# Kernel tuning notes

Measured on AMD Instinct MI355X. Metric: run time of the kernel, lower is better.

Reference implementation:

```python
import jax, jax.numpy as jnp
import numpy as np

B, S, D, H = 2, 2048, 1024, 16
DK = D // H
NEG = -1e9


def setup_inputs() -> dict:
    key = jax.random.key(0)
    ks = jax.random.split(key, 12)
    inp = {
        "query": jax.random.normal(ks[0], (B, S, D), jnp.float32),
        "key": jax.random.normal(ks[1], (B, S, D), jnp.float32),
        "value": jax.random.normal(ks[2], (B, S, D), jnp.float32),
        "mask": jax.random.randint(ks[3], (B, S), 0, 2, jnp.int32),
    }
    # 4 linears (q, k, v, out), each d_model x d_model with bias.
    scale = 1.0 / np.sqrt(D)
    for i, name in enumerate(["wq", "wk", "wv", "wo"]):
        inp[name] = jax.random.uniform(ks[4 + i], (D, D), jnp.float32, -scale, scale)
        inp["b" + name[1]] = jax.random.uniform(ks[8 + i], (D,), jnp.float32, -scale, scale)
    return inp


def _split_heads(x):  # [B,S,D] -> [B,H,S,DK]
    return x.reshape(B, S, H, DK).transpose(0, 2, 1, 3)


def reference(query, key, value, mask, wq, bq, wk, bk, wv, bv, wo, bo):
    q = _split_heads(query @ wq.T + bq)
    k = _split_heads(key @ wk.T + bk)
    v = _split_heads(value @ wv.T + bv)
    scores = jnp.einsum("bhqd,bhkd->bhqk", q, k) / jnp.sqrt(jnp.float32(DK))
    # mask: [B,S] -> [B,1,1,S]; masked_fill where mask == 0
    m = mask[:, None, None, :]
    scores = jnp.where(m == 0, NEG, scores)
    attn = jax.nn.softmax(scores, axis=-1)  # dropout p=0 (eval) -> identity
    x = jnp.einsum("bhqk,bhkd->bhqd", attn, v)
    x = x.transpose(0, 2, 1, 3).reshape(B, S, D)
    return x @ wo.T + bo
```

## Files before the change

### kernel.cpp

```cpp
#include <hip/hip_runtime.h>


typedef _Float16 f16;
typedef _Float16 f16x8 __attribute__((ext_vector_type(8)));
typedef _Float16 f16x4 __attribute__((ext_vector_type(4)));
typedef __fp16 fp16x2r __attribute__((ext_vector_type(2)));
typedef float f32x4 __attribute__((ext_vector_type(4)));

#define MFMA_F16(a, b, c) __builtin_amdgcn_mfma_f32_16x16x32_f16((a), (b), (c), 0, 0, 0)
#define L2E 1.44269504088896340736f

__device__ __forceinline__ void gld16(const void* g, void* l) {
    __builtin_amdgcn_global_load_lds(
        (__attribute__((address_space(1))) void*)(g),
        (__attribute__((address_space(3))) void*)(l), 16, 0, 0);
}

__global__ __launch_bounds__(256) void cvt_kernel(
    const float* __restrict__ q, const float* __restrict__ k,
    const float* __restrict__ v,
    const float* __restrict__ wq, const float* __restrict__ wk,
    const float* __restrict__ wv, const float* __restrict__ wo,
    f16* __restrict__ oq, f16* __restrict__ ok, f16* __restrict__ ov,
    f16* __restrict__ owq, f16* __restrict__ owk, f16* __restrict__ owv,
    f16* __restrict__ owo)
{
    const int z = blockIdx.y;
    const float* src;
    f16* dst;
    int n;
    switch (z) {
        case 0: src = q;  dst = oq;  n = 4194304; break;
        case 1: src = k;  dst = ok;  n = 4194304; break;
        case 2: src = v;  dst = ov;  n = 4194304; break;
        case 3: src = wq; dst = owq; n = 1048576; break;
        case 4: src = wk; dst = owk; n = 1048576; break;
        case 5: src = wv; dst = owv; n = 1048576; break;
        default: src = wo; dst = owo; n = 1048576; break;
    }
    int idx = (blockIdx.x * 256 + threadIdx.x) * 8;
    if (idx >= n) return;
    float4 a = *(const float4*)(src + idx);
    float4 b = *(const float4*)(src + idx + 4);
    f16x8 h = { (f16)a.x, (f16)a.y, (f16)a.z, (f16)a.w,
                (f16)b.x, (f16)b.y, (f16)b.z, (f16)b.w };
    *(f16x8*)(dst + idx) = h;
}

__device__ __forceinline__ void stage_qkv(
    const f16* __restrict__ P0, const f16* __restrict__ P1,
    int blockM, int blockN, int k0, f16* Ad, f16* Bd,
    int wave, int srow2, int schunk)
{
#pragma unroll
    for (int p = 0; p < 2; p++) {
        int r0 = wave * 32 + p * 16;
        gld16(&P0[(size_t)(blockM + r0 + srow2) * 1024 + k0 + schunk * 8],
              &Ad[r0 * 32]);
        gld16(&P1[(size_t)(blockN + r0 + srow2) * 1024 + k0 + schunk * 8],
              &Bd[r0 * 32]);
    }
}

__global__ __launch_bounds__(256) void proj_qkv_kernel(
    const f16* __restrict__ xq, const f16* __restrict__ xk,
    const f16* __restrict__ xv,
    const f16* __restrict__ wqh, const f16* __restrict__ wkh,
    const f16* __restrict__ wvh,
    const float* __restrict__ bq, const float* __restrict__ bk,
    const float* __restrict__ bv,
    f16* __restrict__ qh, f16* __restrict__ kh, f16* __restrict__ vt)
{
    const int z = blockIdx.z;
    const f16* X = (z == 0) ? xq : (z == 1) ? xk : xv;
    const f16* W = (z == 0) ? wqh : (z == 1) ? wkh : wvh;
    const float* bias = (z == 0) ? bq : (z == 1) ? bk : bv;
    const f16* P0 = (z < 2) ? W : X;
    const f16* P1 = (z < 2) ? X : W;

    __shared__ __align__(16) f16 smem[24576];
    f16* L = smem;

    const int t = threadIdx.x;
    const int wave = t >> 6, lane = t & 63, quad = lane >> 4, l15 = lane & 15;
    const int m_base = (wave >> 1) * 64, n_base = (wave & 1) * 64;
    const int blockM = (z < 2) ? blockIdx.y * 128 : blockIdx.x * 128;
    const int blockN = (z < 2) ? blockIdx.x * 128 : blockIdx.y * 128;

    const int srow2 = lane >> 2;
    const int schunk = (lane & 3) ^ ((srow2 >> 1) & 3);
    const int rchunk = (l15 >> 1) & 3;

    f32x4 acc[4][4];
#pragma unroll
    for (int mt = 0; mt < 4; mt++)
#pragma unroll
        for (int nt = 0; nt < 4; nt++)
            acc[mt][nt] = (f32x4){0.f, 0.f, 0.f, 0.f};

    f16 *Ac = smem,          *An = smem + 4096,  *Af = smem + 8192;
    f16 *Bc = smem + 12288,  *Bn = smem + 16384, *Bf = smem + 20480;

    stage_qkv(P0, P1, blockM, blockN, 0,  Ac, Bc, wave, srow2, schunk);
    stage_qkv(P0, P1, blockM, blockN, 32, An, Bn, wave, srow2, schunk);
    asm volatile("s_waitcnt vmcnt(4)" ::: "memory");

    for (int ki = 0; ki < 32; ki++) {
        __builtin_amdgcn_s_barrier();
        __builtin_amdgcn_sched_barrier(0);
        if (ki < 30)
            stage_qkv(P0, P1, blockM, blockN, (ki + 2) * 32, Af, Bf,
                      wave, srow2, schunk);

        f16x8 af[4], bf[4];
#pragma unroll
        for (int mt = 0; mt < 4; mt++)
            af[mt] = *(const f16x8*)(&Ac[(m_base + mt * 16 + l15) * 32 +
                                         ((quad ^ rchunk) << 3)]);
#pragma unroll
        for (int nt = 0; nt < 4; nt++)
            bf[nt] = *(const f16x8*)(&Bc[(n_base + nt * 16 + l15) * 32 +
                                         ((quad ^ rchunk) << 3)]);
        __builtin_amdgcn_s_setprio(1);
#pragma unroll
        for (int mt = 0; mt < 4; mt++)
#pragma unroll
            for (int nt = 0; nt < 4; nt++)
                acc[mt][nt] = MFMA_F16(af[mt], bf[nt], acc[mt][nt]);
        __builtin_amdgcn_s_setprio(0);

        if (ki < 30)
            asm volatile("s_waitcnt vmcnt(4)" ::: "memory");
        else if (ki == 30)
            asm volatile("s_waitcnt vmcnt(0)" ::: "memory");
        f16* tA = Ac; Ac = An; An = Af; Af = tA;
        f16* tB = Bc; Bc = Bn; Bn = Bf; Bf = tB;
    }

    if (z < 2) {
        f16* o = (z == 0) ? qh : kh;
        const float scale = (z == 0) ? 0.125f * L2E : 1.0f;
        float4 b4[4];
#pragma unroll
        for (int mt = 0; mt < 4; mt++)
            b4[mt] = *(const float4*)(&bias[blockM + m_base + mt * 16 + quad * 4]);

#pragma unroll
        for (int half = 0; half < 2; half++) {
            __syncthreads();
            if ((wave & 1) == half) {
#pragma unroll
                for (int mt = 0; mt < 4; mt++)
#pragma unroll
                    for (int nt = 0; nt < 4; nt++) {
                        f16x4 pk = {
                            (f16)((acc[mt][nt][0] + b4[mt].x) * scale),
                            (f16)((acc[mt][nt][1] + b4[mt].y) * scale),
                            (f16)((acc[mt][nt][2] + b4[mt].z) * scale),
                            (f16)((acc[mt][nt][3] + b4[mt].w) * scale) };
                        *(f16x4*)(&L[(nt * 16 + l15) * 136 +
                                     m_base + mt * 16 + quad * 4]) = pk;
                    }
            }
            __syncthreads();
#pragma unroll
            for (int pass = 0; pass < 4; pass++) {
                int unit = pass * 32 + (t >> 3);
                int hh = unit >> 6, s_loc = unit & 63;
                f16x8 vv = *(const f16x8*)(&L[s_loc * 136 + hh * 64 + (t & 7) * 8]);
                int s_glob = blockN + half * 64 + s_loc;
                int b = s_glob >> 11, s = s_glob & 2047;
                int h_glob = (blockM >> 6) + hh;
                *(f16x8*)(&o[(((size_t)(b * 16 + h_glob) * 2048 + s) << 6) +
                             (t & 7) * 8]) = vv;
            }
        }
    } else {
        float bv_[4];
#pragma unroll
        for (int nt = 0; nt < 4; nt++)
            bv_[nt] = bias[blockN + n_base + nt * 16 + l15];

#pragma unroll
        for (int half = 0; half < 2; half++) {
            __syncthreads();
            if ((wave & 1) == half) {
#pragma unroll
                for (int mt = 0; mt < 4; mt++)
#pragma unroll
                    for (int nt = 0; nt < 4; nt++) {
                        f16x4 pk = { (f16)(acc[mt][nt][0] + bv_[nt]),
                                     (f16)(acc[mt][nt][1] + bv_[nt]),
                                     (f16)(acc[mt][nt][2] + bv_[nt]),
                                     (f16)(acc[mt][nt][3] + bv_[nt]) };
                        *(f16x4*)(&L[(nt * 16 + l15) * 136 +
                                     m_base + mt * 16 + quad * 4]) = pk;
                    }
            }
            __syncthreads();
#pragma unroll
            for (int pass = 0; pass < 4; pass++) {
                int f_loc = pass * 16 + (t >> 4);
                int tt = t & 15;
                int bb = (tt >= 8) ? 64 : 0;
                int o  = (tt & 7) * 8;
                int p  = (o >> 5) & 1;
                int c  = (o >> 3) & 3;
                int g1 = bb + p * 32 + c * 4;
                const f16* Lrow = &L[f_loc * 136];
                f16x4 lo = *(const f16x4*)(&Lrow[g1]);
                f16x4 hi = *(const f16x4*)(&Lrow[g1 + 16]);
                f16x8 vv = __builtin_shufflevector(lo, hi, 0, 1, 2, 3, 4, 5, 6, 7);
                int feat = blockN + half * 64 + f_loc;
                int hh = feat >> 6, dk = feat & 63;
                int b = blockM >> 11;
                int s0 = (blockM & 2047) + bb + o;
                *(f16x8*)(&vt[((size_t)((b * 16 + hh) * 64 + dk) << 11) + s0]) = vv;
            }
        }
    }
}

__device__ __forceinline__ void flash_stage2(
    const f16* kbase, const f16* vbase, int key0,
    f16* Kb, f16* Vb, int wg, int srow8, int sblk)
{
#pragma unroll
    for (int p = 0; p < 2; p++) {
        int r0 = wg * 16 + p * 8;
        int row = r0 + srow8;
        gld16(&kbase[(size_t)(key0 + row) * 64 + sblk * 8], &Kb[r0 * 64]);
        gld16(&vbase[(size_t)row * 2048 + key0 + sblk * 8], &Vb[r0 * 64]);
    }
}

__device__ __forceinline__ void flash_phase2(
    const f16* Kbuf, const f16* Vbuf, const float* bias_all, int key0,
    const f16x8 (&qf)[2][2], int quad, int l15,
    f32x4 (&O)[2][4], f32x4 (&lacc)[2])
{
    const int sw = l15 & 7;
    f32x4 sc[2][4];
#pragma unroll
    for (int nt = 0; nt < 4; nt++) {
        const f16* krow = &Kbuf[(nt * 16 + l15) * 64];
        f16x8 kf0 = *(const f16x8*)(&krow[(quad ^ sw) << 3]);
        f16x8 kf1 = *(const f16x8*)(&krow[((quad + 4) ^ sw) << 3]);
        float4 b4 = *(const float4*)(&bias_all[key0 + nt * 16 + quad * 4]);
        __builtin_amdgcn_s_setprio(1);
#pragma unroll
        for (int cb = 0; cb < 2; cb++) {
            f32x4 z4 = (f32x4){b4.x, b4.y, b4.z, b4.w};
            z4 = MFMA_F16(kf0, qf[cb][0], z4);
            sc[cb][nt] = MFMA_F16(kf1, qf[cb][1], z4);
        }
        __builtin_amdgcn_s_setprio(0);
    }
    const f16x8 ones8 = {(f16)1.f, (f16)1.f, (f16)1.f, (f16)1.f,
                         (f16)1.f, (f16)1.f, (f16)1.f, (f16)1.f};
    union P8u { f16x8 v8; fp16x2r h[4]; };
    P8u pp[2][2];
#pragma unroll
    for (int cb = 0; cb < 2; cb++) {
#pragma unroll
        for (int nt = 0; nt < 4; nt++) {
            float p0 = __builtin_amdgcn_exp2f(sc[cb][nt][0]);
            float p1 = __builtin_amdgcn_exp2f(sc[cb][nt][1]);
            float p2 = __builtin_amdgcn_exp2f(sc[cb][nt][2]);
            float p3 = __builtin_amdgcn_exp2f(sc[cb][nt][3]);
            pp[cb][nt >> 1].h[(nt & 1) * 2 + 0] = __builtin_amdgcn_cvt_pkrtz(p0, p1);
            pp[cb][nt >> 1].h[(nt & 1) * 2 + 1] = __builtin_amdgcn_cvt_pkrtz(p2, p3);
        }
        lacc[cb] = MFMA_F16(ones8, pp[cb][0].v8, lacc[cb]);
        lacc[cb] = MFMA_F16(ones8, pp[cb][1].v8, lacc[cb]);
    }
    __builtin_amdgcn_s_setprio(1);
#pragma unroll
    for (int nto = 0; nto < 4; nto++) {
        const f16* vrow = &Vbuf[(nto * 16 + l15) * 64];
        f16x8 va = *(const f16x8*)(&vrow[(quad ^ sw) << 3]);
        f16x8 vb = *(const f16x8*)(&vrow[((4 + quad) ^ sw) << 3]);
#pragma unroll
        for (int cb = 0; cb < 2; cb++) {
            O[cb][nto] = MFMA_F16(va, pp[cb][0].v8, O[cb][nto]);
            O[cb][nto] = MFMA_F16(vb, pp[cb][1].v8, O[cb][nto]);
        }
    }
    __builtin_amdgcn_s_setprio(0);
}

__global__
__attribute__((amdgpu_flat_work_group_size(512, 512)))
__attribute__((amdgpu_waves_per_eu(4, 4)))
void flash_kernel(
    const f16* __restrict__ qh, const f16* __restrict__ kh,
    const f16* __restrict__ vt, const int* __restrict__ mask,
    f16* __restrict__ ctx)
{
    __shared__ __align__(16) f16 KV[8 * 4096];
    __shared__ float bias_all[2048];

    const int t = threadIdx.x;
    const int wave = t >> 6, lane = t & 63, quad = lane >> 4, l15 = lane & 15;
    const int group = wave >> 2, wg = wave & 3;
    const int bh = blockIdx.x;
    const int b = bh >> 4, h = bh & 15;
    const int q0 = blockIdx.y * 128;

    const f16* qbase = qh + (size_t)bh * (2048 * 64);
    const f16* kbase = kh + (size_t)bh * (2048 * 64);
    const f16* vbase = vt + (size_t)bh * (64 * 2048);

    f16* K0 = &KV[((0 * 2 + group) * 2 + 0) * 4096];
    f16* V0 = &KV[((0 * 2 + group) * 2 + 1) * 4096];
    f16* K1 = &KV[((1 * 2 + group) * 2 + 0) * 4096];
    f16* V1 = &KV[((1 * 2 + group) * 2 + 1) * 4096];

#pragma unroll
    for (int j = 0; j < 4; j++) {
        int i = j * 512 + t;
        bias_all[i] = (mask[b * 2048 + i] == 0) ? -1.0e9f : 0.0f;
    }

    f16x8 qf[2][2];
#pragma unroll
    for (int cb = 0; cb < 2; cb++) {
        int qrow = q0 + wg * 32 + cb * 16 + l15;
        qf[cb][0] = *(const f16x8*)(&qbase[qrow * 64 + quad * 8]);
        qf[cb][1] = *(const f16x8*)(&qbase[qrow * 64 + 32 + quad * 8]);
    }

    f32x4 O[2][4];
#pragma unroll
    for (int cb = 0; cb < 2; cb++)
#pragma unroll
        for (int n = 0; n < 4; n++) O[cb][n] = (f32x4){0.f, 0.f, 0.f, 0.f};
    f32x4 lacc[2] = {(f32x4){0.f, 0.f, 0.f, 0.f}, (f32x4){0.f, 0.f, 0.f, 0.f}};

    const int srow8 = lane >> 3;
    const int sblk = (lane & 7) ^ srow8;

    flash_stage2(kbase, vbase, group * 64, K0, V0, wg, srow8, sblk);

    for (int k2 = 0; k2 < 16; k2 += 2) {
        __syncthreads();
        flash_stage2(kbase, vbase, (k2 + 1) * 128 + group * 64, K1, V1,
                     wg, srow8, sblk);
        flash_phase2(K0, V0, bias_all, k2 * 128 + group * 64,
                     qf, quad, l15, O, lacc);
        __syncthreads();
        if (k2 < 14)
            flash_stage2(kbase, vbase, (k2 + 2) * 128 + group * 64, K0, V0,
                         wg, srow8, sblk);
        flash_phase2(K1, V1, bias_all, (k2 + 1) * 128 + group * 64,
                     qf, quad, l15, O, lacc);
    }

    __syncthreads();
    float* Red = (float*)KV;
    const int t4 = wg * 64 + lane;
    if (group == 1) {
#pragma unroll
        for (int cb = 0; cb < 2; cb++) {
#pragma unroll
            for (int nto = 0; nto < 4; nto++)
                *(f32x4*)(&Red[(cb * 4 + nto) * 1024 + t4 * 4]) = O[cb][nto];
            Red[8 * 1024 + cb * 256 + t4] = lacc[cb][0];
        }
    }
    __syncthreads();
    if (group == 0) {
#pragma unroll
        for (int cb = 0; cb < 2; cb++) {
            const float l2 = Red[8 * 1024 + cb * 256 + t4];
            const float inv_l = 1.0f / (lacc[cb][0] + l2);
            int qrow = q0 + wg * 32 + cb * 16 + l15;
#pragma unroll
            for (int nto = 0; nto < 4; nto++) {
                f32x4 o2 = *(const f32x4*)(&Red[(cb * 4 + nto) * 1024 + t4 * 4]);
                f16x4 pk = { (f16)((O[cb][nto][0] + o2[0]) * inv_l),
                             (f16)((O[cb][nto][1] + o2[1]) * inv_l),
                             (f16)((O[cb][nto][2] + o2[2]) * inv_l),
                             (f16)((O[cb][nto][3] + o2[3]) * inv_l) };
                *(f16x4*)(&ctx[(size_t)(b * 2048 + qrow) * 1024 + h * 64 +
                               nto * 16 + quad * 4]) = pk;
            }
        }
    }
}

__device__ __forceinline__ void stage_out(
    const f16* __restrict__ ctx, const f16* __restrict__ woh,
    int blockM, int blockN, int k0, f16* Ad, f16* Bd,
    int wave, int srow2, int schunk)
{
#pragma unroll
    for (int p = 0; p < 2; p++) {
        int r0 = wave * 32 + p * 16;
        gld16(&ctx[(size_t)(blockM + r0 + srow2) * 1024 + k0 + schunk * 8],
              &Ad[r0 * 32]);
    }
    {
        int r0 = wave * 16;
        gld16(&woh[(size_t)(blockN + r0 + srow2) * 1024 + k0 + schunk * 8],
              &Bd[r0 * 32]);
    }
}

__global__ __launch_bounds__(256) void proj_out_kernel(
    const f16* __restrict__ ctx, const f16* __restrict__ woh,
    const float* __restrict__ bo, float* __restrict__ out)
{
    __shared__ __align__(16) f16 smem[18432];

    const int t = threadIdx.x;
    const int wave = t >> 6, lane = t & 63, quad = lane >> 4, l15 = lane & 15;
    const int m_base = (wave >> 1) * 64, n_base = (wave & 1) * 32;
    const int blockM = blockIdx.x * 128;
    const int blockN = blockIdx.y * 64;

    const int srow2 = lane >> 2;
    const int schunk = (lane & 3) ^ ((srow2 >> 1) & 3);
    const int rchunk = (l15 >> 1) & 3;

    f32x4 acc[4][2];
#pragma unroll
    for (int mt = 0; mt < 4; mt++)
#pragma unroll
        for (int nt = 0; nt < 2; nt++)
            acc[mt][nt] = (f32x4){0.f, 0.f, 0.f, 0.f};

    f16 *Ac = smem,          *An = smem + 4096,  *Af = smem + 8192;
    f16 *Bc = smem + 12288,  *Bn = smem + 14336, *Bf = smem + 16384;

    stage_out(ctx, woh, blockM, blockN, 0,  Ac, Bc, wave, srow2, schunk);
    stage_out(ctx, woh, blockM, blockN, 32, An, Bn, wave, srow2, schunk);
    asm volatile("s_waitcnt vmcnt(3)" ::: "memory");

    for (int ki = 0; ki < 32; ki++) {
        __builtin_amdgcn_s_barrier();
        __builtin_amdgcn_sched_barrier(0);
        if (ki < 30)
            stage_out(ctx, woh, blockM, blockN, (ki + 2) * 32, Af, Bf,
                      wave, srow2, schunk);

        f16x8 af[4], bf[2];
#pragma unroll
        for (int mt = 0; mt < 4; mt++)
            af[mt] = *(const f16x8*)(&Ac[(m_base + mt * 16 + l15) * 32 +
                                         ((quad ^ rchunk) << 3)]);
#pragma unroll
        for (int nt = 0; nt < 2; nt++)
            bf[nt] = *(const f16x8*)(&Bc[(n_base + nt * 16 + l15) * 32 +
                                         ((quad ^ rchunk) << 3)]);
        __builtin_amdgcn_s_setprio(1);
#pragma unroll
        for (int mt = 0; mt < 4; mt++)
#pragma unroll
            for (int nt = 0; nt < 2; nt++)
                acc[mt][nt] = MFMA_F16(af[mt], bf[nt], acc[mt][nt]);
        __builtin_amdgcn_s_setprio(0);

        if (ki < 30)
            asm volatile("s_waitcnt vmcnt(3)" ::: "memory");
        else if (ki == 30)
            asm volatile("s_waitcnt vmcnt(0)" ::: "memory");
        f16* tA = Ac; Ac = An; An = Af; Af = tA;
        f16* tB = Bc; Bc = Bn; Bn = Bf; Bf = tB;
    }

    float bo_[2];
#pragma unroll
    for (int nt = 0; nt < 2; nt++)
        bo_[nt] = bo[blockN + n_base + nt * 16 + l15];

#pragma unroll
    for (int mt = 0; mt < 4; mt++) {
        int row0 = blockM + m_base + mt * 16 + quad * 4;
#pragma unroll
        for (int nt = 0; nt < 2; nt++) {
            int col_g = blockN + n_base + nt * 16 + l15;
#pragma unroll
            for (int i = 0; i < 4; i++)
                out[(size_t)(row0 + i) * 1024 + col_g] = acc[mt][nt][i] + bo_[nt];
        }
    }
}

extern "C" void kernel_launch(void* const* d_in, const int* in_sizes, int n_in,
                              void* d_out, int out_size, void* d_ws, size_t ws_size,
                              hipStream_t stream) {
    const float* query = (const float*)d_in[0];
    const float* key_  = (const float*)d_in[1];
    const float* value = (const float*)d_in[2];
    const int*   mask  = (const int*)d_in[3];
    const float* wq = (const float*)d_in[4];
    const float* bq = (const float*)d_in[5];
    const float* wk = (const float*)d_in[6];
    const float* bk = (const float*)d_in[7];
    const float* wv = (const float*)d_in[8];
    const float* bv = (const float*)d_in[9];
    const float* wo = (const float*)d_in[10];
    const float* bo = (const float*)d_in[11];
    float* out = (float*)d_out;

    f16* xq  = (f16*)d_ws;
    f16* xk  = xq  + 4194304;
    f16* xv  = xk  + 4194304;
    f16* wqh = xv  + 4194304;
    f16* wkh = wqh + 1048576;
    f16* wvh = wkh + 1048576;
    f16* woh = wvh + 1048576;
    f16* qh  = woh + 1048576;
    f16* kh  = qh  + 4194304;
    f16* vt  = kh  + 4194304;
    f16* ctx = xq;

    cvt_kernel<<<dim3(2048, 7), 256, 0, stream>>>(
        query, key_, value, wq, wk, wv, wo, xq, xk, xv, wqh, wkh, wvh, woh);
    proj_qkv_kernel<<<dim3(32, 8, 3), 256, 0, stream>>>(
        xq, xk, xv, wqh, wkh, wvh, bq, bk, bv, qh, kh, vt);
    flash_kernel<<<dim3(32, 16), 512, 0, stream>>>(qh, kh, vt, mask, ctx);
    proj_out_kernel<<<dim3(32, 16), 256, 0, stream>>>(ctx, woh, bo, out);
}
```

Before: 209.6 us.

## Replace MFMA row-sum with scalar accumulation and retile output projection

```diff
diff --git a/kernel.cpp b/kernel.cpp
--- a/kernel.cpp
+++ b/kernel.cpp
@@ -237,7 +237,7 @@
 __device__ __forceinline__ void flash_phase2(
     const f16* Kbuf, const f16* Vbuf, const float* bias_all, int key0,
     const f16x8 (&qf)[2][2], int quad, int l15,
-    f32x4 (&O)[2][4], f32x4 (&lacc)[2])
+    f32x4 (&O)[2][4], float (&lsum)[2])
 {
     const int sw = l15 & 7;
     f32x4 sc[2][4];
@@ -256,12 +256,11 @@
         }
         __builtin_amdgcn_s_setprio(0);
     }
-    const f16x8 ones8 = {(f16)1.f, (f16)1.f, (f16)1.f, (f16)1.f,
-                         (f16)1.f, (f16)1.f, (f16)1.f, (f16)1.f};
     union P8u { f16x8 v8; fp16x2r h[4]; };
     P8u pp[2][2];
 #pragma unroll
     for (int cb = 0; cb < 2; cb++) {
+        float lacc = 0.f;
 #pragma unroll
         for (int nt = 0; nt < 4; nt++) {
             float p0 = __builtin_amdgcn_exp2f(sc[cb][nt][0]);
@@ -270,9 +269,9 @@
             float p3 = __builtin_amdgcn_exp2f(sc[cb][nt][3]);
             pp[cb][nt >> 1].h[(nt & 1) * 2 + 0] = __builtin_amdgcn_cvt_pkrtz(p0, p1);
             pp[cb][nt >> 1].h[(nt & 1) * 2 + 1] = __builtin_amdgcn_cvt_pkrtz(p2, p3);
-        }
-        lacc[cb] = MFMA_F16(ones8, pp[cb][0].v8, lacc[cb]);
-        lacc[cb] = MFMA_F16(ones8, pp[cb][1].v8, lacc[cb]);
+            lacc += (p0 + p1) + (p2 + p3);
+        }
+        lsum[cb] += lacc;
     }
     __builtin_amdgcn_s_setprio(1);
 #pragma unroll
@@ -335,7 +334,7 @@
     for (int cb = 0; cb < 2; cb++)
 #pragma unroll
         for (int n = 0; n < 4; n++) O[cb][n] = (f32x4){0.f, 0.f, 0.f, 0.f};
-    f32x4 lacc[2] = {(f32x4){0.f, 0.f, 0.f, 0.f}, (f32x4){0.f, 0.f, 0.f, 0.f}};
+    float lsum[2] = {0.f, 0.f};
 
     const int srow8 = lane >> 3;
     const int sblk = (lane & 7) ^ srow8;
@@ -347,13 +346,21 @@
         flash_stage2(kbase, vbase, (k2 + 1) * 128 + group * 64, K1, V1,
                      wg, srow8, sblk);
         flash_phase2(K0, V0, bias_all, k2 * 128 + group * 64,
-                     qf, quad, l15, O, lacc);
+                     qf, quad, l15, O, lsum);
         __syncthreads();
         if (k2 < 14)
             flash_stage2(kbase, vbase, (k2 + 2) * 128 + group * 64, K0, V0,
                          wg, srow8, sblk);
         flash_phase2(K1, V1, bias_all, (k2 + 1) * 128 + group * 64,
-                     qf, quad, l15, O, lacc);
+                     qf, quad, l15, O, lsum);
+    }
+
+#pragma unroll
+    for (int cb = 0; cb < 2; cb++) {
+        float v = lsum[cb];
+        v += __shfl_xor(v, 16, 64);
+        v += __shfl_xor(v, 32, 64);
+        lsum[cb] = v;
     }
 
     __syncthreads();
@@ -365,7 +372,7 @@
 #pragma unroll
             for (int nto = 0; nto < 4; nto++)
                 *(f32x4*)(&Red[(cb * 4 + nto) * 1024 + t4 * 4]) = O[cb][nto];
-            Red[8 * 1024 + cb * 256 + t4] = lacc[cb][0];
+            Red[8 * 1024 + cb * 256 + t4] = lsum[cb];
         }
     }
     __syncthreads();
@@ -373,7 +380,7 @@
 #pragma unroll
         for (int cb = 0; cb < 2; cb++) {
             const float l2 = Red[8 * 1024 + cb * 256 + t4];
-            const float inv_l = 1.0f / (lacc[cb][0] + l2);
+            const float inv_l = 1.0f / (lsum[cb] + l2);
             int qrow = q0 + wg * 32 + cb * 16 + l15;
 #pragma unroll
             for (int nto = 0; nto < 4; nto++) {
@@ -392,18 +399,15 @@
 __device__ __forceinline__ void stage_out(
     const f16* __restrict__ ctx, const f16* __restrict__ woh,
     int blockM, int blockN, int k0, f16* Ad, f16* Bd,
-    int wave, int srow2, int schunk)
+    int wave, int srow8, int sblk)
 {
 #pragma unroll
     for (int p = 0; p < 2; p++) {
-        int r0 = wave * 32 + p * 16;
-        gld16(&ctx[(size_t)(blockM + r0 + srow2) * 1024 + k0 + schunk * 8],
-              &Ad[r0 * 32]);
-    }
-    {
-        int r0 = wave * 16;
-        gld16(&woh[(size_t)(blockN + r0 + srow2) * 1024 + k0 + schunk * 8],
-              &Bd[r0 * 32]);
+        int r0 = wave * 16 + p * 8;
+        gld16(&ctx[(size_t)(blockM + r0 + srow8) * 1024 + k0 + sblk * 8],
+              &Ad[r0 * 64]);
+        gld16(&woh[(size_t)(blockN + r0 + srow8) * 1024 + k0 + sblk * 8],
+              &Bd[r0 * 64]);
     }
 }
 
@@ -411,62 +415,61 @@
     const f16* __restrict__ ctx, const f16* __restrict__ woh,
     const float* __restrict__ bo, float* __restrict__ out)
 {
-    __shared__ __align__(16) f16 smem[18432];
+    __shared__ __align__(16) f16 smem[16384];
 
     const int t = threadIdx.x;
     const int wave = t >> 6, lane = t & 63, quad = lane >> 4, l15 = lane & 15;
-    const int m_base = (wave >> 1) * 64, n_base = (wave & 1) * 32;
-    const int blockM = blockIdx.x * 128;
+    const int m_base = (wave >> 1) * 32, n_base = (wave & 1) * 32;
+    const int blockM = blockIdx.x * 64;
     const int blockN = blockIdx.y * 64;
 
-    const int srow2 = lane >> 2;
-    const int schunk = (lane & 3) ^ ((srow2 >> 1) & 3);
-    const int rchunk = (l15 >> 1) & 3;
-
-    f32x4 acc[4][2];
-#pragma unroll
-    for (int mt = 0; mt < 4; mt++)
+    const int srow8 = lane >> 3;
+    const int sblk = (lane & 7) ^ srow8;
+
+    f32x4 acc[2][2];
+#pragma unroll
+    for (int mt = 0; mt < 2; mt++)
 #pragma unroll
         for (int nt = 0; nt < 2; nt++)
             acc[mt][nt] = (f32x4){0.f, 0.f, 0.f, 0.f};
 
-    f16 *Ac = smem,          *An = smem + 4096,  *Af = smem + 8192;
-    f16 *Bc = smem + 12288,  *Bn = smem + 14336, *Bf = smem + 16384;
-
-    stage_out(ctx, woh, blockM, blockN, 0,  Ac, Bc, wave, srow2, schunk);
-    stage_out(ctx, woh, blockM, blockN, 32, An, Bn, wave, srow2, schunk);
-    asm volatile("s_waitcnt vmcnt(3)" ::: "memory");
-
-    for (int ki = 0; ki < 32; ki++) {
+    f16 *Ac = smem,         *An = smem + 4096;
+    f16 *Bc = smem + 8192,  *Bn = smem + 12288;
+
+    stage_out(ctx, woh, blockM, blockN, 0, Ac, Bc, wave, srow8, sblk);
+    asm volatile("s_waitcnt vmcnt(0)" ::: "memory");
+
+    for (int ki = 0; ki < 16; ki++) {
         __builtin_amdgcn_s_barrier();
         __builtin_amdgcn_sched_barrier(0);
-        if (ki < 30)
-            stage_out(ctx, woh, blockM, blockN, (ki + 2) * 32, Af, Bf,
-                      wave, srow2, schunk);
-
-        f16x8 af[4], bf[2];
-#pragma unroll
-        for (int mt = 0; mt < 4; mt++)
-            af[mt] = *(const f16x8*)(&Ac[(m_base + mt * 16 + l15) * 32 +
-                                         ((quad ^ rchunk) << 3)]);
-#pragma unroll
-        for (int nt = 0; nt < 2; nt++)
-            bf[nt] = *(const f16x8*)(&Bc[(n_base + nt * 16 + l15) * 32 +
-                                         ((quad ^ rchunk) << 3)]);
-        __builtin_amdgcn_s_setprio(1);
-#pragma unroll
-        for (int mt = 0; mt < 4; mt++)
+        if (ki < 15)
+            stage_out(ctx, woh, blockM, blockN, (ki + 1) * 64, An, Bn,
+                      wave, srow8, sblk);
+
+#pragma unroll
+        for (int kc = 0; kc < 2; kc++) {
+            f16x8 af[2], bf[2];
+#pragma unroll
+            for (int mt = 0; mt < 2; mt++)
+                af[mt] = *(const f16x8*)(&Ac[(m_base + mt * 16 + l15) * 64 +
+                                             (((kc * 4 + quad) ^ (l15 & 7)) << 3)]);
 #pragma unroll
             for (int nt = 0; nt < 2; nt++)
-                acc[mt][nt] = MFMA_F16(af[mt], bf[nt], acc[mt][nt]);
-        __builtin_amdgcn_s_setprio(0);
-
-        if (ki < 30)
-            asm volatile("s_waitcnt vmcnt(3)" ::: "memory");
-        else if (ki == 30)
+                bf[nt] = *(const f16x8*)(&Bc[(n_base + nt * 16 + l15) * 64 +
+                                             (((kc * 4 + quad) ^ (l15 & 7)) << 3)]);
+            __builtin_amdgcn_s_setprio(1);
+#pragma unroll
+            for (int mt = 0; mt < 2; mt++)
+#pragma unroll
+                for (int nt = 0; nt < 2; nt++)
+                    acc[mt][nt] = MFMA_F16(af[mt], bf[nt], acc[mt][nt]);
+            __builtin_amdgcn_s_setprio(0);
+        }
+
+        if (ki < 15)
             asm volatile("s_waitcnt vmcnt(0)" ::: "memory");
-        f16* tA = Ac; Ac = An; An = Af; Af = tA;
-        f16* tB = Bc; Bc = Bn; Bn = Bf; Bf = tB;
+        f16* tA = Ac; Ac = An; An = tA;
+        f16* tB = Bc; Bc = Bn; Bn = tB;
     }
 
     float bo_[2];
@@ -475,7 +478,7 @@
         bo_[nt] = bo[blockN + n_base + nt * 16 + l15];
 
 #pragma unroll
-    for (int mt = 0; mt < 4; mt++) {
+    for (int mt = 0; mt < 2; mt++) {
         int row0 = blockM + m_base + mt * 16 + quad * 4;
 #pragma unroll
         for (int nt = 0; nt < 2; nt++) {
@@ -521,5 +524,5 @@
     proj_qkv_kernel<<<dim3(32, 8, 3), 256, 0, stream>>>(
         xq, xk, xv, wqh, wkh, wvh, bq, bk, bv, qh, kh, vt);
     flash_kernel<<<dim3(32, 16), 512, 0, stream>>>(qh, kh, vt, mask, ctx);
-    proj_out_kernel<<<dim3(32, 16), 256, 0, stream>>>(ctx, woh, bo, out);
-}
+    proj_out_kernel<<<dim3(64, 16), 256, 0, stream>>>(ctx, woh, bo, out);
+}
```

After: 221.0 us. 1.05x slower.
